# Performance work log

Hardware: AMD Instinct MI355X
Metric: run time of the kernel (lower is better)

Reference implementation:

```python
import jax, jax.numpy as jnp
import numpy as np

PI = float(np.pi)


def _apply_acts(a, x):
    """Vectorized per-node activation dispatch.
    a: [n] int activation ids (applyAct lookup table), x: [B, n].
    Matches torch applyAct: ids 2..11 select a function, anything else is identity.
    """
    A = a[None, :]  # broadcast over batch
    v = x  # actId 1 / default: identity
    v = jnp.where(A == 2, (x > 0.0).astype(x.dtype), v)           # unsigned step
    v = jnp.where(A == 3, jnp.sin(PI * x), v)                      # sin
    v = jnp.where(A == 4, jnp.exp(-0.5 * x * x), v)                # gaussian
    v = jnp.where(A == 5, jnp.tanh(x), v)                          # tanh
    v = jnp.where(A == 6, 0.5 * (jnp.tanh(0.5 * x) + 1.0), v)      # sigmoid
    v = jnp.where(A == 7, -x, v)                                   # inverse
    v = jnp.where(A == 8, jnp.abs(x), v)                           # abs
    v = jnp.where(A == 9, jnp.maximum(0.0, x), v)                  # relu
    v = jnp.where(A == 10, jnp.cos(PI * x), v)                     # cos
    v = jnp.where(A == 11, x * x, v)                               # squared
    return v


def setup_inputs() -> dict:
    key = jax.random.key(0)
    ks = jax.random.split(key, 10)
    B, nIn, H1, H2, nOut = 65536, 256, 256, 256, 128
    SPARSITY = 0.5  # fraction of zeroed connections, like a WANN sparse topology

    def sparse_w(kw, km, shape):
        w = jax.random.normal(kw, shape, jnp.float32)
        keep = jax.random.uniform(km, shape) > SPARSITY
        return w * keep.astype(jnp.float32)

    x = jax.random.normal(ks[0], (B, nIn), jnp.float32)
    W0 = sparse_w(ks[1], ks[2], (nIn + 1, H1))  # layer0 (bias+inputs) -> layer1
    W1 = sparse_w(ks[3], ks[4], (H1, H2))       # layer1 -> layer2
    W2 = sparse_w(ks[5], ks[6], (H2, nOut))     # layer2 -> output layer
    a1 = jax.random.randint(ks[7], (H1,), 0, 12).astype(jnp.int32)
    a2 = jax.random.randint(ks[8], (H2,), 0, 12).astype(jnp.int32)
    a3 = jax.random.randint(ks[9], (nOut,), 0, 12).astype(jnp.int32)
    return {"x": x, "W0": W0, "W1": W1, "W2": W2, "a1": a1, "a2": a2, "a3": a3}


def reference(x, W0, W1, W2, a1, a2, a3):
    B = x.shape[0]
    # layer 0 activations: bias node (=1) followed by the inputs
    h = jnp.concatenate([jnp.ones((B, 1), x.dtype), x], axis=1)  # [B, nIn+1]
    # each SparseLinear is (weight * mask) matmul; mask = weight != 0
    h = _apply_acts(a1, h @ (W0 * (W0 != 0)))  # [B, H1]
    h = _apply_acts(a2, h @ (W1 * (W1 != 0)))  # [B, H2]
    h = _apply_acts(a3, h @ (W2 * (W2 != 0)))  # [B, nOut]
    return h  # all_activations[:, -nOutput:] == final layer
```

## Files before the change

kernel.cpp:

```cpp
#include <hip/hip_runtime.h>
#include <hip/hip_bf16.h>
#include <math.h>

typedef __attribute__((ext_vector_type(8)))  short short8;
typedef __attribute__((ext_vector_type(16))) float f32x16;

constexpr int TB = 32;
constexpr int PLANE = 16384;

__device__ __forceinline__ float vexp2f(float x) {
    float r; asm("v_exp_f32 %0, %1" : "=v"(r) : "v"(x)); return r;
}

__device__ __forceinline__ unsigned int cvtpk_bf16(float a, float b) {
    unsigned int r;
    asm("v_cvt_pk_bf16_f32 %0, %1, %2" : "=v"(r) : "v"(a), "v"(b));
    return r;
}

__device__ __forceinline__ void split3_pair(float v0, float v1,
                                            unsigned int& hp, unsigned int& mp, unsigned int& lp) {
    hp = cvtpk_bf16(v0, v1);
    const float h0 = __uint_as_float(hp << 16);
    const float h1 = __uint_as_float(hp & 0xffff0000u);
    const float r0 = v0 - h0, r1 = v1 - h1;
    mp = cvtpk_bf16(r0, r1);
    const float m0 = __uint_as_float(mp << 16);
    const float m1 = __uint_as_float(mp & 0xffff0000u);
    lp = cvtpk_bf16(r0 - m0, r1 - m1);
}

__device__ __forceinline__ unsigned int bf16_rne_bits(float x) {
    unsigned int u = __float_as_uint(x);
    return (u + 0x7fffu + ((u >> 16) & 1u)) & 0xffff0000u;
}
__device__ __forceinline__ void split3(float x, unsigned short& h, unsigned short& m, unsigned short& l) {
    const unsigned int hb = bf16_rne_bits(x);
    const float r1 = x - __uint_as_float(hb);
    const unsigned int mb = bf16_rne_bits(r1);
    const float r2 = r1 - __uint_as_float(mb);
    h = (unsigned short)(hb >> 16);
    m = (unsigned short)(mb >> 16);
    l = (unsigned short)(__float_as_uint(r2) >> 16);
}

__device__ __forceinline__ float apply_act(int a, float x) {
    const float x2 = x * x;
    const float roff = (a == 10) ? 0.25f : 0.0f;
    const float r  = __builtin_amdgcn_fractf(fmaf(0.5f, x, roff));
    const float sn = __builtin_amdgcn_sinf(r);
    const float eop = (a == 4) ? x2 : x;
    const float ecf = (a == 4) ? -0.72134752044448169f
                               : ((a == 5) ? 2.8853900817779268f : -1.4426950408889634f);
    const float e  = vexp2f(eop * ecf);
    const float d  = __builtin_amdgcn_rcpf(1.0f + e);
    float ev = d;
    ev = (a == 4) ? e : ev;
    ev = (a == 5) ? fmaf(-2.0f, d, 1.0f) : ev;
    float v = x;
    v = (a == 2)  ? (x > 0.0f ? 1.0f : 0.0f) : v;
    v = (a == 3 || a == 10) ? sn : v;
    v = (a >= 4 && a <= 6)  ? ev : v;
    v = (a == 7)  ? -x : v;
    v = (a == 8)  ? fabsf(x) : v;
    v = (a == 9)  ? fmaxf(0.0f, x) : v;
    v = (a == 11) ? x2 : v;
    return v;
}

__global__ void pack_w(const float* __restrict__ W0, const float* __restrict__ W1,
                       const float* __restrict__ W2, unsigned short* __restrict__ ws) {
    const int g = blockIdx.x * 4 + (threadIdx.x >> 6);
    const int lane = threadIdx.x & 63;
    const int hi = lane >> 5, ln31 = lane & 31;
    const float* W; int t, c, ldw, rowoff;
    if (g < 128)      { W = W0; t = g >> 3;        c = g & 7;        ldw = 256; rowoff = 1; }
    else if (g < 256) { W = W1; t = (g-128) >> 3;  c = (g-128) & 7;  ldw = 256; rowoff = 0; }
    else              { W = W2; t = (g-256) >> 2;  c = (g-256) & 3;  ldw = 128; rowoff = 0; }
    const int col = c * 32 + ln31;
    unsigned short hb[8], mb[8], lb[8];
    #pragma unroll
    for (int i = 0; i < 8; ++i) {
        const int k = t * 16 + hi * 8 + i;
        split3(W[(size_t)(rowoff + k) * ldw + col], hb[i], mb[i], lb[i]);
    }
    size_t base = ((size_t)(g * 3 + 0) * 64 + lane) * 8;
    #pragma unroll
    for (int i = 0; i < 8; ++i) ws[base + i] = hb[i];
    base += 64 * 8;
    #pragma unroll
    for (int i = 0; i < 8; ++i) ws[base + i] = mb[i];
    base += 64 * 8;
    #pragma unroll
    for (int i = 0; i < 8; ++i) ws[base + i] = lb[i];
}

template<int NC_TOT>
__device__ __forceinline__ void gemm_layer(const short8* __restrict__ wsL, const char* smem,
                                           f32x16& acc, int ctile, int lane) {
    const int hi = lane >> 5, ln31 = lane & 31;
    const int abase = ln31 * 512;
    const int swzm = (ln31 & 7) << 4;
    const short8* bp = wsL + (size_t)ctile * 192 + lane;
    #pragma unroll 2
    for (int t = 0; t < 16; ++t) {
        const int koff = abase + ((t * 32 + hi * 16) ^ swzm);
        short8 ah = *(const short8*)(smem + 0 * PLANE + koff);
        short8 am = *(const short8*)(smem + 1 * PLANE + koff);
        short8 al = *(const short8*)(smem + 2 * PLANE + koff);
        short8 bh = bp[0];
        short8 bm = bp[64];
        short8 bl = bp[128];
        bp += NC_TOT * 192;
        __builtin_amdgcn_s_setprio(1);
        acc = __builtin_amdgcn_mfma_f32_32x32x16_bf16(ah, bh, acc, 0, 0, 0);
        acc = __builtin_amdgcn_mfma_f32_32x32x16_bf16(ah, bm, acc, 0, 0, 0);
        acc = __builtin_amdgcn_mfma_f32_32x32x16_bf16(am, bh, acc, 0, 0, 0);
        acc = __builtin_amdgcn_mfma_f32_32x32x16_bf16(ah, bl, acc, 0, 0, 0);
        acc = __builtin_amdgcn_mfma_f32_32x32x16_bf16(am, bm, acc, 0, 0, 0);
        acc = __builtin_amdgcn_mfma_f32_32x32x16_bf16(al, bh, acc, 0, 0, 0);
        __builtin_amdgcn_s_setprio(0);
    }
}

__device__ __forceinline__ void act_store_lds(f32x16& acc, const int* __restrict__ act,
                                              char* smem, int ctile, int lane) {
    const int hi = lane >> 5, ln31 = lane & 31;
    const int col = ctile * 32 + ln31;
    const int aid = act[col];
    const int kbyte = 2 * col;
    #pragma unroll
    for (int rr = 0; rr < 16; ++rr) acc[rr] = apply_act(aid, acc[rr]);
    __syncthreads();
    #pragma unroll
    for (int p = 0; p < 8; ++p) {
        const int rr0 = 2 * p;
        unsigned int hp, mp, lp;
        split3_pair(acc[rr0], acc[rr0 + 1], hp, mp, lp);
        const int row0 = (rr0 & 3) + 8 * (rr0 >> 2) + 4 * hi;
        const int a0 = row0 * 512 + (kbyte ^ ((row0 & 7) << 4));
        const int a1 = (row0 + 1) * 512 + (kbyte ^ (((row0 + 1) & 7) << 4));
        *(unsigned short*)(smem + 0 * PLANE + a0) = (unsigned short)hp;
        *(unsigned short*)(smem + 0 * PLANE + a1) = (unsigned short)(hp >> 16);
        *(unsigned short*)(smem + 1 * PLANE + a0) = (unsigned short)mp;
        *(unsigned short*)(smem + 1 * PLANE + a1) = (unsigned short)(mp >> 16);
        *(unsigned short*)(smem + 2 * PLANE + a0) = (unsigned short)lp;
        *(unsigned short*)(smem + 2 * PLANE + a1) = (unsigned short)(lp >> 16);
    }
    __syncthreads();
}

__global__ __launch_bounds__(512, 6)
void wann_mfma(const float* __restrict__ x,
               const float* __restrict__ W0,
               const unsigned short* __restrict__ ws,
               const int* __restrict__ a1, const int* __restrict__ a2,
               const int* __restrict__ a3,
               float* __restrict__ out) {
    extern __shared__ char smem[];
    const int tid = threadIdx.x;
    const int lane = tid & 63;
    const int wid = tid >> 6;
    const int ln31 = lane & 31;
    const int hi = lane >> 5;
    const int row0 = blockIdx.x * TB;

    {
        const float4* xv = (const float4*)(x + (size_t)row0 * 256);
        #pragma unroll
        for (int p = 0; p < 4; ++p) {
            const int f = p * 512 + tid;
            const int r = f >> 6;
            const int swz = (r & 7) << 4;
            const int kb0 = (f & 63) * 8;
            const float4 v = xv[f];
            unsigned int h01, m01, l01, h23, m23, l23;
            split3_pair(v.x, v.y, h01, m01, l01);
            split3_pair(v.z, v.w, h23, m23, l23);
            const int a0 = r * 512 + (kb0 ^ swz);
            *(unsigned long long*)(smem + 0 * PLANE + a0) =
                (unsigned long long)h01 | ((unsigned long long)h23 << 32);
            *(unsigned long long*)(smem + 1 * PLANE + a0) =
                (unsigned long long)m01 | ((unsigned long long)m23 << 32);
            *(unsigned long long*)(smem + 2 * PLANE + a0) =
                (unsigned long long)l01 | ((unsigned long long)l23 << 32);
        }
    }
    __syncthreads();

    const short8* wsv  = (const short8*)ws;
    const short8* wsL0 = wsv;
    const short8* wsL1 = wsv + (size_t)128 * 3 * 64;
    const short8* wsL2 = wsv + (size_t)256 * 3 * 64;

    f32x16 acc;

    {
        const float b = W0[wid * 32 + ln31];
        #pragma unroll
        for (int rr = 0; rr < 16; ++rr) acc[rr] = b;
        gemm_layer<8>(wsL0, smem, acc, wid, lane);
        act_store_lds(acc, a1, smem, wid, lane);
    }

    {
        #pragma unroll
        for (int rr = 0; rr < 16; ++rr) acc[rr] = 0.0f;
        gemm_layer<8>(wsL1, smem, acc, wid, lane);
        act_store_lds(acc, a2, smem, wid, lane);
    }

    if (wid < 4) {
        #pragma unroll
        for (int rr = 0; rr < 16; ++rr) acc[rr] = 0.0f;
        gemm_layer<4>(wsL2, smem, acc, wid, lane);
        const int col = wid * 32 + ln31;
        const int aid = a3[col];
        #pragma unroll
        for (int rr = 0; rr < 16; ++rr) {
            const float v = apply_act(aid, acc[rr]);
            const int orow = (rr & 3) + 8 * (rr >> 2) + 4 * hi;
            out[(size_t)(row0 + orow) * 128 + col] = v;
        }
    }
}

extern "C" void kernel_launch(void* const* d_in, const int* in_sizes, int n_in,
                              void* d_out, int out_size, void* d_ws, size_t ws_size,
                              hipStream_t stream) {
    const float* x  = (const float*)d_in[0];
    const float* W0 = (const float*)d_in[1];
    const float* W1 = (const float*)d_in[2];
    const float* W2 = (const float*)d_in[3];
    const int*   a1 = (const int*)d_in[4];
    const int*   a2 = (const int*)d_in[5];
    const int*   a3 = (const int*)d_in[6];
    float* out = (float*)d_out;

    unsigned short* ws = (unsigned short*)d_ws;

    hipFuncSetAttribute(reinterpret_cast<const void*>(wann_mfma),
                        hipFuncAttributeMaxDynamicSharedMemorySize, 3 * PLANE);

    hipLaunchKernelGGL(pack_w, dim3(80), dim3(256), 0, stream, W0, W1, W2, ws);

    const int B = in_sizes[0] / 256;
    hipLaunchKernelGGL(wann_mfma, dim3(B / TB), dim3(512), 3 * PLANE, stream,
                       x, W0, ws, a1, a2, a3, out);
}
```

Measured before the change: 239.7 us.

## Split final layer K across all waves and prefetch first weight tiles

The final 128-column layer now uses all eight waves: each pair of waves splits the K dimension in half, and the partial accumulators are summed through LDS before the activation and store. The first weight fragment of each layer is loaded early, before the preceding sync or input staging, to hide global latency. The trailing sync in act_store_lds is moved so it comes after those prefetches, and the s_setprio hints are removed. This adds an LDS reduction and extra barriers in exchange for not leaving half the waves idle in layer three.

```diff
diff --git a/kernel.cpp b/kernel.cpp
--- a/kernel.cpp
+++ b/kernel.cpp
@@ -95,31 +95,42 @@
     for (int i = 0; i < 8; ++i) ws[base + i] = lb[i];
 }
 
-template<int NC_TOT>
+template<int NC_TOT, int NKT>
 __device__ __forceinline__ void gemm_layer(const short8* __restrict__ wsL, const char* smem,
-                                           f32x16& acc, int ctile, int lane) {
+                                           f32x16& acc, int ctile, int lane, int t0,
+                                           short8 bh, short8 bm, short8 bl) {
     const int hi = lane >> 5, ln31 = lane & 31;
     const int abase = ln31 * 512;
     const int swzm = (ln31 & 7) << 4;
-    const short8* bp = wsL + (size_t)ctile * 192 + lane;
-    #pragma unroll 2
-    for (int t = 0; t < 16; ++t) {
-        const int koff = abase + ((t * 32 + hi * 16) ^ swzm);
+    {
+        const int koff = abase + ((t0 * 32 + hi * 16) ^ swzm);
         short8 ah = *(const short8*)(smem + 0 * PLANE + koff);
         short8 am = *(const short8*)(smem + 1 * PLANE + koff);
         short8 al = *(const short8*)(smem + 2 * PLANE + koff);
-        short8 bh = bp[0];
-        short8 bm = bp[64];
-        short8 bl = bp[128];
-        bp += NC_TOT * 192;
-        __builtin_amdgcn_s_setprio(1);
         acc = __builtin_amdgcn_mfma_f32_32x32x16_bf16(ah, bh, acc, 0, 0, 0);
         acc = __builtin_amdgcn_mfma_f32_32x32x16_bf16(ah, bm, acc, 0, 0, 0);
         acc = __builtin_amdgcn_mfma_f32_32x32x16_bf16(am, bh, acc, 0, 0, 0);
         acc = __builtin_amdgcn_mfma_f32_32x32x16_bf16(ah, bl, acc, 0, 0, 0);
         acc = __builtin_amdgcn_mfma_f32_32x32x16_bf16(am, bm, acc, 0, 0, 0);
         acc = __builtin_amdgcn_mfma_f32_32x32x16_bf16(al, bh, acc, 0, 0, 0);
-        __builtin_amdgcn_s_setprio(0);
+    }
+    const short8* bp = wsL + ((size_t)(t0 + 1) * NC_TOT + ctile) * 192 + lane;
+    #pragma unroll 2
+    for (int t = t0 + 1; t < t0 + NKT; ++t) {
+        const int koff = abase + ((t * 32 + hi * 16) ^ swzm);
+        short8 ah = *(const short8*)(smem + 0 * PLANE + koff);
+        short8 am = *(const short8*)(smem + 1 * PLANE + koff);
+        short8 al = *(const short8*)(smem + 2 * PLANE + koff);
+        short8 cbh = bp[0];
+        short8 cbm = bp[64];
+        short8 cbl = bp[128];
+        bp += NC_TOT * 192;
+        acc = __builtin_amdgcn_mfma_f32_32x32x16_bf16(ah, cbh, acc, 0, 0, 0);
+        acc = __builtin_amdgcn_mfma_f32_32x32x16_bf16(ah, cbm, acc, 0, 0, 0);
+        acc = __builtin_amdgcn_mfma_f32_32x32x16_bf16(am, cbh, acc, 0, 0, 0);
+        acc = __builtin_amdgcn_mfma_f32_32x32x16_bf16(ah, cbl, acc, 0, 0, 0);
+        acc = __builtin_amdgcn_mfma_f32_32x32x16_bf16(am, cbm, acc, 0, 0, 0);
+        acc = __builtin_amdgcn_mfma_f32_32x32x16_bf16(al, cbh, acc, 0, 0, 0);
     }
 }
 
@@ -147,7 +158,6 @@
         *(unsigned short*)(smem + 2 * PLANE + a0) = (unsigned short)lp;
         *(unsigned short*)(smem + 2 * PLANE + a1) = (unsigned short)(lp >> 16);
     }
-    __syncthreads();
 }
 
 __global__ __launch_bounds__(512, 6)
@@ -164,6 +174,14 @@
     const int ln31 = lane & 31;
     const int hi = lane >> 5;
     const int row0 = blockIdx.x * TB;
+
+    const short8* wsv  = (const short8*)ws;
+    const short8* wsL0 = wsv;
+    const short8* wsL1 = wsv + (size_t)128 * 3 * 64;
+    const short8* wsL2 = wsv + (size_t)256 * 3 * 64;
+
+    const short8* p0 = wsL0 + (size_t)wid * 192 + lane;
+    short8 b0h = p0[0], b0m = p0[64], b0l = p0[128];
 
     {
         const float4* xv = (const float4*)(x + (size_t)row0 * 256);
@@ -188,33 +206,54 @@
     }
     __syncthreads();
 
-    const short8* wsv  = (const short8*)ws;
-    const short8* wsL0 = wsv;
-    const short8* wsL1 = wsv + (size_t)128 * 3 * 64;
-    const short8* wsL2 = wsv + (size_t)256 * 3 * 64;
-
     f32x16 acc;
 
     {
         const float b = W0[wid * 32 + ln31];
         #pragma unroll
         for (int rr = 0; rr < 16; ++rr) acc[rr] = b;
-        gemm_layer<8>(wsL0, smem, acc, wid, lane);
+        gemm_layer<8, 16>(wsL0, smem, acc, wid, lane, 0, b0h, b0m, b0l);
         act_store_lds(acc, a1, smem, wid, lane);
     }
+    const short8* p1 = wsL1 + (size_t)wid * 192 + lane;
+    short8 b1h = p1[0], b1m = p1[64], b1l = p1[128];
+    __syncthreads();
 
     {
         #pragma unroll
         for (int rr = 0; rr < 16; ++rr) acc[rr] = 0.0f;
-        gemm_layer<8>(wsL1, smem, acc, wid, lane);
+        gemm_layer<8, 16>(wsL1, smem, acc, wid, lane, 0, b1h, b1m, b1l);
         act_store_lds(acc, a2, smem, wid, lane);
     }
-
-    if (wid < 4) {
+    const int c3 = wid & 3, kh = wid >> 2, t0 = kh * 8;
+    const short8* p2 = wsL2 + ((size_t)(t0 * 4 + c3)) * 192 + lane;
+    short8 b2h = p2[0], b2m = p2[64], b2l = p2[128];
+    __syncthreads();
+
+    {
         #pragma unroll
         for (int rr = 0; rr < 16; ++rr) acc[rr] = 0.0f;
-        gemm_layer<4>(wsL2, smem, acc, wid, lane);
-        const int col = wid * 32 + ln31;
+        gemm_layer<4, 8>(wsL2, smem, acc, c3, lane, t0, b2h, b2m, b2l);
+    }
+    __syncthreads();
+    float* red = (float*)smem;
+    if (kh == 1) {
+        const int base = ((wid - 4) * 64 + lane) * 16;
+        #pragma unroll
+        for (int q = 0; q < 4; ++q) {
+            float4 v = make_float4(acc[4*q], acc[4*q+1], acc[4*q+2], acc[4*q+3]);
+            *(float4*)(red + base + 4 * q) = v;
+        }
+    }
+    __syncthreads();
+    if (kh == 0) {
+        const int base = (wid * 64 + lane) * 16;
+        #pragma unroll
+        for (int q = 0; q < 4; ++q) {
+            const float4 v = *(const float4*)(red + base + 4 * q);
+            acc[4*q] += v.x; acc[4*q+1] += v.y; acc[4*q+2] += v.z; acc[4*q+3] += v.w;
+        }
+        const int col = c3 * 32 + ln31;
         const int aid = a3[col];
         #pragma unroll
         for (int rr = 0; rr < 16; ++rr) {
```

Result: faster. 224.5 us (-6.3%).
